# Optimization experiments

Hardware: AMD Instinct MI355X
Metric: run time of the kernel (lower is better)

Reference implementation:

```python
import jax, jax.numpy as jnp
import numpy as np


def _conv(x, w, b, pad):
    y = jax.lax.conv_general_dilated(x, w, window_strides=(1, 1),
                                     padding=[(pad, pad), (pad, pad)],
                                     dimension_numbers=('NCHW', 'OIHW', 'NCHW'))
    return y + b[None, :, None, None]


def _kernel_normalizer(mask, k):
    # softmax over the k*k kernel taps; hamming=1 so the renorm is a numerical no-op (kept faithful)
    n, mck2, h, w = mask.shape
    mc = mck2 // (k * k)
    m = jax.nn.softmax(mask.reshape(n, mc, k * k, h, w), axis=2)
    m = m / jnp.sum(m, axis=2, keepdims=True)
    return m.reshape(n, mck2, h, w)


def _carafe(feat, mask, k, g, s):
    # CARAFE: out[n,c,i,j] = sum_{ki,kj} mask[n, grp*k*k + ki*k + kj, i, j] * feat[n, c, i//s+ki-r, j//s+kj-r]
    n, c, h, w = feat.shape
    r = (k - 1) // 2
    cg = c // g
    hs, ws = h * s, w * s
    pad = jnp.pad(feat, ((0, 0), (0, 0), (r, r), (r, r)))
    m = mask.reshape(n, g, k * k, hs, ws)
    out = jnp.zeros((n, g, cg, hs, ws), feat.dtype)
    idx = 0
    for ki in range(k):
        for kj in range(k):
            sh = pad[:, :, ki:ki + h, kj:kj + w]
            if s > 1:
                sh = jnp.repeat(jnp.repeat(sh, s, axis=2), s, axis=3)
            out = out + sh.reshape(n, g, cg, hs, ws) * m[:, :, idx][:, :, None]
            idx += 1
    return out.reshape(n, c, hs, ws)


def setup_inputs() -> dict:
    key = jax.random.key(0)
    ks = jax.random.split(key, 8)
    N, CH, CL, H, W, CC = 4, 256, 256, 128, 128, 64
    KL, KH, EK = 5, 3, 3

    def w_init(k, shape):
        fan_in = shape[1] * shape[2] * shape[3]
        return jax.random.normal(k, shape, jnp.float32) * (1.0 / np.sqrt(fan_in))

    return {
        'hr_feat': jax.random.normal(ks[0], (N, CH, H, W), jnp.float32),
        'lr_feat': jax.random.normal(ks[1], (N, CL, H // 2, W // 2), jnp.float32),
        'hr_w': w_init(ks[2], (CC, CH, 1, 1)), 'hr_b': jnp.zeros((CC,), jnp.float32),
        'lr_w': w_init(ks[3], (CC, CL, 1, 1)), 'lr_b': jnp.zeros((CC,), jnp.float32),
        'enc_w': w_init(ks[4], (KL * KL, CC, EK, EK)), 'enc_b': jnp.zeros((KL * KL,), jnp.float32),
        'enc2_w': w_init(ks[5], (KH * KH, CC, EK, EK)), 'enc2_b': jnp.zeros((KH * KH,), jnp.float32),
    }


def reference(hr_feat, lr_feat, hr_w, hr_b, lr_w, lr_b, enc_w, enc_b, enc2_w, enc2_b):
    KL, KH, G = 5, 3, 1
    chf = _conv(hr_feat, hr_w, hr_b, 0)
    clf = _conv(lr_feat, lr_w, lr_b, 0)
    mask_hr_hr = _conv(chf, enc2_w, enc2_b, 1)
    mask_hr_init = _kernel_normalizer(mask_hr_hr, KH)
    chf = chf + chf - _carafe(chf, mask_hr_init, KH, G, 1)
    mask_lr_hr = _conv(chf, enc_w, enc_b, 1)
    mask_lr_init = _kernel_normalizer(mask_lr_hr, KL)
    mask_lr_lr_lr = _conv(clf, enc_w, enc_b, 1)
    # carafe scale-2 output is already hr-sized -> F.interpolate(nearest, hr size) is identity
    mask_lr_lr = _carafe(mask_lr_lr_lr, mask_lr_init, KL, G, 2)
    mask_lr = mask_lr_hr + mask_lr_lr
    mask_lr_init = _kernel_normalizer(mask_lr, KL)
    mask_hr_lr = _carafe(_conv(clf, enc2_w, enc2_b, 1), mask_lr_init, KL, G, 2)
    mask_hr = mask_hr_hr + mask_hr_lr
    mask_lr_out = _kernel_normalizer(mask_lr, KL)
    lr_out = _carafe(lr_feat, mask_lr_out, KL, G, 2)
    mask_hr_out = _kernel_normalizer(mask_hr, KH)
    hr_out = (hr_feat - _carafe(hr_feat, mask_hr_out, KH, G, 1)) + hr_feat
    return (mask_lr_out, hr_out, lr_out)
```

## Files before the change

### kernel.cpp

```cpp
#include <hip/hip_runtime.h>
#include <hip/hip_bf16.h>

typedef __hip_bfloat16 bf16;

constexpr int Nn  = 4;
constexpr int Ci  = 256;
constexpr int Cc  = 64;
constexpr int Hh  = 128;
constexpr int Ww  = 128;
constexpr int HWh = Hh * Ww;
constexpr int Hl  = 64;
constexpr int Wl  = 64;
constexpr int HWl = Hl * Wl;
constexpr int K2L = 25;
constexpr int K2H = 9;

constexpr size_t OFF_MASK = 0;
constexpr size_t OFF_HR   = (size_t)Nn * K2L * HWh;
constexpr size_t OFF_LR   = OFF_HR + (size_t)Nn * Ci * HWh;

constexpr size_t A_CHF    = 0;
constexpr size_t A_MLRHR  = 0;
constexpr size_t A_MLRLL  = 1700000;
constexpr size_t A_CLFE2  = 2200000;
constexpr size_t A_MLRS1  = 2400000;
constexpr size_t A_MHR2S  = 4100000;
constexpr size_t A_WHR    = 7800000;
constexpr size_t A_WLR    = 7820000;
constexpr size_t A_WENC   = 7840000;
constexpr size_t A_WENC2  = 7860000;
constexpr size_t A_BHR    = 7870000;
constexpr size_t A_BLR    = 7870100;
constexpr size_t A_BENC   = 7870200;
constexpr size_t A_BENC2  = 7870300;

constexpr size_t B_CLF    = 0;
constexpr size_t B_CHF2   = 1100000;
constexpr size_t B_MHRHR  = 5300000;
constexpr size_t B_MHRSM  = 5900000;
constexpr size_t B_MLR    = 0;
constexpr size_t B_MHR2   = 1700000;

__device__ __forceinline__ float tofloat(float v) { return v; }
__device__ __forceinline__ float tofloat(bf16 v) { return __bfloat162float(v); }

template<typename T> __device__ __forceinline__ T fromfloat(float v);
template<> __device__ __forceinline__ float fromfloat<float>(float v) { return v; }
template<> __device__ __forceinline__ bf16  fromfloat<bf16>(float v)  { return __float2bfloat16(v); }

__device__ __forceinline__ float* scrp(void* d, int f32, size_t reg, size_t off) {
  float* b = f32 ? ((float*)d + reg) : (float*)((bf16*)d + reg);
  return b + off;
}

__global__ void detect_dtype(const void* feat, int* flag) {
  __shared__ int s;
  if (threadIdx.x == 0) s = 0;
  __syncthreads();
  unsigned short b = ((const unsigned short*)feat)[threadIdx.x];
  float v = __uint_as_float(((unsigned int)b) << 16);
  if (!(fabsf(v) < 1000.0f)) atomicOr(&s, 1);
  __syncthreads();
  if (threadIdx.x == 0) *flag = s;
}

template<typename T>
__device__ void prep_body(const T* hw, const T* hb, const T* lw, const T* lb,
                          const T* ew, const T* eb, const T* e2w, const T* e2b,
                          float* whr, float* wlr, float* wenc, float* wenc2,
                          float* bhr, float* blr, float* benc, float* benc2) {
  int tid = blockIdx.x * 256 + threadIdx.x, nt = gridDim.x * 256;
  for (int i = tid; i < Cc * Ci; i += nt) {
    int co = i / Ci, ci = i % Ci;
    whr[ci * Cc + co] = tofloat(hw[i]);
    wlr[ci * Cc + co] = tofloat(lw[i]);
  }
  for (int i = tid; i < K2L * Cc * 9; i += nt) {
    int ko = i / (Cc * 9), r = i % (Cc * 9), ci = r / 9, k = r % 9;
    wenc[(ci * K2L + ko) * 9 + k] = tofloat(ew[i]);
  }
  for (int i = tid; i < K2H * Cc * 9; i += nt) {
    int ko = i / (Cc * 9), r = i % (Cc * 9), ci = r / 9, k = r % 9;
    wenc2[(ci * K2H + ko) * 9 + k] = tofloat(e2w[i]);
  }
  if (tid < Cc)  { bhr[tid] = tofloat(hb[tid]); blr[tid] = tofloat(lb[tid]); }
  if (tid < K2L) benc[tid]  = tofloat(eb[tid]);
  if (tid < K2H) benc2[tid] = tofloat(e2b[tid]);
}

__global__ void prep_weights(const int* flag, void* dout,
                             const void* hw, const void* hb, const void* lw, const void* lb,
                             const void* ew, const void* eb, const void* e2w, const void* e2b) {
  int f32 = *flag;
  float* whr   = scrp(dout, f32, OFF_LR, A_WHR);
  float* wlr   = scrp(dout, f32, OFF_LR, A_WLR);
  float* wenc  = scrp(dout, f32, OFF_LR, A_WENC);
  float* wenc2 = scrp(dout, f32, OFF_LR, A_WENC2);
  float* bhr   = scrp(dout, f32, OFF_LR, A_BHR);
  float* blr   = scrp(dout, f32, OFF_LR, A_BLR);
  float* benc  = scrp(dout, f32, OFF_LR, A_BENC);
  float* benc2 = scrp(dout, f32, OFF_LR, A_BENC2);
  if (f32) prep_body<float>((const float*)hw, (const float*)hb, (const float*)lw, (const float*)lb,
                            (const float*)ew, (const float*)eb, (const float*)e2w, (const float*)e2b,
                            whr, wlr, wenc, wenc2, bhr, blr, benc, benc2);
  else     prep_body<bf16>((const bf16*)hw, (const bf16*)hb, (const bf16*)lw, (const bf16*)lb,
                           (const bf16*)ew, (const bf16*)eb, (const bf16*)e2w, (const bf16*)e2b,
                           whr, wlr, wenc, wenc2, bhr, blr, benc, benc2);
}

template<typename T>
__device__ void conv1x1_body(const T* __restrict__ in, const float* __restrict__ wt,
                             const float* __restrict__ bias, float* __restrict__ out, int P) {
  const int tid = threadIdx.x;
  const int n = blockIdx.y;
  const int pbase = blockIdx.x * 64 + (tid & 63);
  const int co0 = __builtin_amdgcn_readfirstlane((tid >> 6) << 4);
  const T* inp = in + (size_t)n * Ci * P + pbase;

  float acc[16];
  #pragma unroll
  for (int c = 0; c < 16; ++c) acc[c] = bias[co0 + c];

  #pragma unroll 4
  for (int ci = 0; ci < Ci; ++ci) {
    float v = tofloat(inp[(size_t)ci * P]);
    const float* wr = wt + ci * Cc + co0;
    #pragma unroll
    for (int c = 0; c < 16; ++c) acc[c] = fmaf(v, wr[c], acc[c]);
  }
  float* op = out + (size_t)n * Cc * P + pbase;
  #pragma unroll
  for (int c = 0; c < 16; ++c) op[(size_t)(co0 + c) * P] = acc[c];
}

__global__ __launch_bounds__(256) void conv1x1_k(const int* flag, void* dout, const void* in,
                                                 size_t w_off, size_t b_off,
                                                 size_t o_reg, size_t o_off, int P) {
  int f32 = __builtin_amdgcn_readfirstlane(*flag);
  const float* wt   = scrp(dout, f32, OFF_LR, w_off);
  const float* bias = scrp(dout, f32, OFF_LR, b_off);
  float* out        = scrp(dout, f32, o_reg, o_off);
  if (f32) conv1x1_body<float>((const float*)in, wt, bias, out, P);
  else     conv1x1_body<bf16>((const bf16*)in, wt, bias, out, P);
}

template<int KO, int KOG>
__global__ __launch_bounds__(256) void conv3x3_k(const int* flag, void* dout,
                                                 size_t i_reg, size_t i_off,
                                                 size_t w_off, size_t b_off,
                                                 size_t o_reg, size_t o_off, int hh, int ww) {
  const int f32 = __builtin_amdgcn_readfirstlane(*flag);
  const float* in   = scrp(dout, f32, i_reg, i_off);
  const float* wt   = scrp(dout, f32, OFF_LR, w_off);
  const float* bias = scrp(dout, f32, OFF_LR, b_off);
  float* out        = scrp(dout, f32, o_reg, o_off);

  constexpr int NG = KO / KOG;
  __shared__ float tile[16 * 18 * 18];
  const int tid = threadIdx.x;
  const int tx = tid & 15, ty = tid >> 4;
  const int bx = blockIdx.x * 16, by = blockIdx.y * 16;
  const int n = blockIdx.z / NG;
  const int ko0 = (blockIdx.z % NG) * KOG;

  float acc[KOG];
  #pragma unroll
  for (int ko = 0; ko < KOG; ++ko) acc[ko] = bias[ko0 + ko];

  for (int cc = 0; cc < Cc; cc += 16) {
    __syncthreads();
    for (int i = tid; i < 16 * 18 * 18; i += 256) {
      int ci = i / 324, r = i % 324, yy = r / 18, xx = r % 18;
      int gy = by + yy - 1, gx = bx + xx - 1;
      float v = 0.f;
      if (gy >= 0 && gy < hh && gx >= 0 && gx < ww)
        v = in[(((size_t)n * Cc + cc + ci) * hh + gy) * ww + gx];
      tile[i] = v;
    }
    __syncthreads();
    for (int ci = 0; ci < 16; ++ci) {
      float nb[9];
      #pragma unroll
      for (int dy = 0; dy < 3; ++dy)
        #pragma unroll
        for (int dx = 0; dx < 3; ++dx)
          nb[dy * 3 + dx] = tile[ci * 324 + (ty + dy) * 18 + tx + dx];
      const float* wr = wt + ((size_t)(cc + ci) * KO + ko0) * 9;
      #pragma unroll
      for (int ko = 0; ko < KOG; ++ko)
        #pragma unroll
        for (int k = 0; k < 9; ++k)
          acc[ko] = fmaf(wr[ko * 9 + k], nb[k], acc[ko]);
    }
  }
  const size_t ob = (((size_t)n * KO + ko0) * hh + by + ty) * ww + bx + tx;
  #pragma unroll
  for (int ko = 0; ko < KOG; ++ko) out[ob + (size_t)ko * hh * ww] = acc[ko];
}

template<int K2>
__global__ __launch_bounds__(256) void softmax_k(const int* flag, void* dout,
                                                 size_t i_reg, size_t i_off,
                                                 int wf32, size_t o_reg, size_t o_off, int w0) {
  int f32 = __builtin_amdgcn_readfirstlane(*flag);
  const float* in = scrp(dout, f32, i_reg, i_off);
  const int p = blockIdx.x * blockDim.x + threadIdx.x;
  const int n = blockIdx.y;
  const float* ip = in + (size_t)n * K2 * HWh + p;
  float v[K2], m = -1e30f;
  #pragma unroll
  for (int k = 0; k < K2; ++k) { v[k] = ip[(size_t)k * HWh]; m = fmaxf(m, v[k]); }
  float s = 0.f;
  #pragma unroll
  for (int k = 0; k < K2; ++k) { v[k] = __expf(v[k] - m); s += v[k]; }
  const float inv = 1.0f / s;
  #pragma unroll
  for (int k = 0; k < K2; ++k) v[k] *= inv;

  if (wf32) {
    float* op = scrp(dout, f32, o_reg, o_off) + (size_t)n * K2 * HWh + p;
    #pragma unroll
    for (int k = 0; k < K2; ++k) op[(size_t)k * HWh] = v[k];
  }
  if (w0) {
    const size_t g = (size_t)n * K2 * HWh + p;
    if (f32) {
      float* o = (float*)dout;
      #pragma unroll
      for (int k = 0; k < K2; ++k) o[g + (size_t)k * HWh] = v[k];
    } else {
      bf16* o = (bf16*)dout;
      #pragma unroll
      for (int k = 0; k < K2; ++k) o[g + (size_t)k * HWh] = fromfloat<bf16>(v[k]);
    }
  }
}

template<typename FT, typename OT, int FINAL>
__device__ void carafe1_body(const FT* __restrict__ feat, const float* __restrict__ mask,
                             void* dout, size_t out_reg, float* outscr, int C, int CPB) {
  const int tid = threadIdx.x;
  const int tx = tid & 15, ty = tid >> 4;
  const int bx = blockIdx.x * 16, by = blockIdx.y * 16;
  const int numCG = C / CPB;
  const int n = blockIdx.z / numCG, cg = blockIdx.z % numCG;
  const int x = bx + tx, y = by + ty;

  float mv[9];
  #pragma unroll
  for (int k = 0; k < 9; ++k)
    mv[k] = mask[(((size_t)n * 9 + k) * Hh + y) * Ww + x];

  const int c0 = cg * CPB;
  for (int c = c0; c < c0 + CPB; ++c) {
    const FT* fp = feat + ((size_t)n * C + c) * HWh;
    float s = 0.f, center = 0.f;
    #pragma unroll
    for (int dy = -1; dy <= 1; ++dy)
      #pragma unroll
      for (int dx = -1; dx <= 1; ++dx) {
        int yy = y + dy, xx = x + dx;
        float fv = 0.f;
        if (yy >= 0 && yy < Hh && xx >= 0 && xx < Ww) fv = tofloat(fp[yy * Ww + xx]);
        if (dy == 0 && dx == 0) center = fv;
        s = fmaf(fv, mv[(dy + 1) * 3 + (dx + 1)], s);
      }
    float r = 2.f * center - s;
    const size_t li = ((size_t)n * C + c) * HWh + y * Ww + x;
    if (FINAL) ((OT*)dout)[out_reg + li] = fromfloat<OT>(r);
    else       outscr[li] = r;
  }
}

__global__ __launch_bounds__(256) void carafe1_scr_k(const int* flag, void* dout,
    size_t f_reg, size_t f_off, size_t m_reg, size_t m_off, size_t o_reg, size_t o_off,
    int C, int CPB) {
  int f32 = __builtin_amdgcn_readfirstlane(*flag);
  carafe1_body<float, float, 0>(scrp(dout, f32, f_reg, f_off), scrp(dout, f32, m_reg, m_off),
                                dout, 0, scrp(dout, f32, o_reg, o_off), C, CPB);
}

__global__ __launch_bounds__(256) void carafe1_io_k(const int* flag, void* dout, const void* feat,
    size_t m_reg, size_t m_off, size_t out_reg, int C, int CPB) {
  int f32 = __builtin_amdgcn_readfirstlane(*flag);
  const float* m = scrp(dout, f32, m_reg, m_off);
  if (f32) carafe1_body<float, float, 1>((const float*)feat, m, dout, out_reg, nullptr, C, CPB);
  else     carafe1_body<bf16, bf16, 1>((const bf16*)feat, m, dout, out_reg, nullptr, C, CPB);
}

template<typename FT, typename MT, typename OT, int ADD, int FINAL>
__device__ void carafe2_body(const FT* __restrict__ feat, const MT* __restrict__ mask,
                             const float* __restrict__ addend, void* dout, size_t out_reg,
                             float* outscr, int C, int CPB) {
  __shared__ float ft[8][144];
  const int tid = threadIdx.x;
  const int tx = tid & 15, ty = tid >> 4;
  const int bx = blockIdx.x * 16, by = blockIdx.y * 16;
  const int numCG = C / CPB;
  const int n = blockIdx.z / numCG, cg = blockIdx.z % numCG;
  const int x = bx + tx, y = by + ty;

  float mv[25];
  #pragma unroll
  for (int k = 0; k < 25; ++k)
    mv[k] = tofloat(mask[(((size_t)n * 25 + k) * Hh + y) * Ww + x]);

  const int fy0 = (by >> 1) - 2, fx0 = (bx >> 1) - 2;
  const int fyb = (ty >> 1) + 2, fxb = (tx >> 1) + 2;
  const int c0 = cg * CPB;

  for (int cb = 0; cb < CPB; cb += 8) {
    const int lim = (CPB - cb < 8) ? (CPB - cb) : 8;
    __syncthreads();
    for (int i = tid; i < lim * 144; i += 256) {
      int cc = i / 144, r = i % 144, fy = r / 12, fx = r % 12;
      int gy = fy0 + fy, gx = fx0 + fx;
      float v = 0.f;
      if (gy >= 0 && gy < Hl && gx >= 0 && gx < Wl)
        v = tofloat(feat[((size_t)n * C + c0 + cb + cc) * HWl + gy * Wl + gx]);
      ft[cc][r] = v;
    }
    __syncthreads();
    for (int cc = 0; cc < lim; ++cc) {
      float s = 0.f;
      #pragma unroll
      for (int ki = 0; ki < 5; ++ki)
        #pragma unroll
        for (int kj = 0; kj < 5; ++kj)
          s = fmaf(ft[cc][(fyb + ki - 2) * 12 + (fxb + kj - 2)], mv[ki * 5 + kj], s);
      const size_t li = (((size_t)n * C + c0 + cb + cc) * Hh + y) * Ww + x;
      float r = ADD ? (addend[li] + s) : s;
      if (FINAL) ((OT*)dout)[out_reg + li] = fromfloat<OT>(r);
      else       outscr[li] = r;
    }
  }
}

__global__ __launch_bounds__(256) void carafe2_scr_k(const int* flag, void* dout,
    size_t f_reg, size_t f_off, size_t m_reg, size_t m_off, size_t a_reg, size_t a_off,
    size_t o_reg, size_t o_off, int C, int CPB) {
  int f32 = __builtin_amdgcn_readfirstlane(*flag);
  carafe2_body<float, float, float, 1, 0>(scrp(dout, f32, f_reg, f_off), scrp(dout, f32, m_reg, m_off),
      scrp(dout, f32, a_reg, a_off), dout, 0, scrp(dout, f32, o_reg, o_off), C, CPB);
}

__global__ __launch_bounds__(256) void carafe2_m0_k(const int* flag, void* dout,
    size_t f_reg, size_t f_off, size_t a_reg, size_t a_off, size_t o_reg, size_t o_off,
    int C, int CPB) {
  int f32 = __builtin_amdgcn_readfirstlane(*flag);
  const float* f = scrp(dout, f32, f_reg, f_off);
  const float* a = scrp(dout, f32, a_reg, a_off);
  float* o = scrp(dout, f32, o_reg, o_off);
  if (f32) carafe2_body<float, float, float, 1, 0>(f, (const float*)dout, a, dout, 0, o, C, CPB);
  else     carafe2_body<float, bf16, float, 1, 0>(f, (const bf16*)dout, a, dout, 0, o, C, CPB);
}

__global__ __launch_bounds__(256) void carafe2_io_k(const int* flag, void* dout, const void* feat,
    size_t out_reg, int C, int CPB) {
  int f32 = __builtin_amdgcn_readfirstlane(*flag);
  if (f32) carafe2_body<float, float, float, 0, 1>((const float*)feat, (const float*)dout,
      nullptr, dout, out_reg, nullptr, C, CPB);
  else     carafe2_body<bf16, bf16, bf16, 0, 1>((const bf16*)feat, (const bf16*)dout,
      nullptr, dout, out_reg, nullptr, C, CPB);
}

extern "C" void kernel_launch(void* const* d_in, const int* in_sizes, int n_in,
                              void* d_out, int out_size, void* d_ws, size_t ws_size,
                              hipStream_t stream) {
  const void* hr_feat = d_in[0];
  const void* lr_feat = d_in[1];
  int* flag = (int*)d_ws;

  detect_dtype<<<1, 256, 0, stream>>>(hr_feat, flag);
  prep_weights<<<64, 256, 0, stream>>>(flag, d_out, d_in[2], d_in[3], d_in[4], d_in[5],
                                       d_in[6], d_in[7], d_in[8], d_in[9]);
  conv1x1_k<<<dim3(HWh / 64, Nn), 256, 0, stream>>>(flag, d_out, hr_feat, A_WHR, A_BHR, OFF_LR, A_CHF, HWh);
  conv1x1_k<<<dim3(HWl / 64, Nn), 256, 0, stream>>>(flag, d_out, lr_feat, A_WLR, A_BLR, OFF_HR, B_CLF, HWl);
  conv3x3_k<K2H, 3><<<dim3(8, 8, Nn * 3), 256, 0, stream>>>(flag, d_out, OFF_LR, A_CHF, A_WENC2, A_BENC2, OFF_HR, B_MHRHR, Hh, Ww);
  softmax_k<K2H><<<dim3(HWh / 128, Nn), 128, 0, stream>>>(flag, d_out, OFF_HR, B_MHRHR, 1, OFF_HR, B_MHRSM, 0);
  carafe1_scr_k<<<dim3(8, 8, Nn * (Cc / 16)), 256, 0, stream>>>(flag, d_out, OFF_LR, A_CHF, OFF_HR, B_MHRSM, OFF_HR, B_CHF2, Cc, 16);
  conv3x3_k<K2L, 5><<<dim3(8, 8, Nn * 5), 256, 0, stream>>>(flag, d_out, OFF_HR, B_CHF2, A_WENC, A_BENC, OFF_LR, A_MLRHR, Hh, Ww);
  conv3x3_k<K2L, 5><<<dim3(4, 4, Nn * 5), 256, 0, stream>>>(flag, d_out, OFF_HR, B_CLF, A_WENC, A_BENC, OFF_LR, A_MLRLL, Hl, Wl);
  conv3x3_k<K2H, 3><<<dim3(4, 4, Nn * 3), 256, 0, stream>>>(flag, d_out, OFF_HR, B_CLF, A_WENC2, A_BENC2, OFF_LR, A_CLFE2, Hl, Wl);
  softmax_k<K2L><<<dim3(HWh / 128, Nn), 128, 0, stream>>>(flag, d_out, OFF_LR, A_MLRHR, 1, OFF_LR, A_MLRS1, 0);
  carafe2_scr_k<<<dim3(8, 8, Nn * 5), 256, 0, stream>>>(flag, d_out, OFF_LR, A_MLRLL, OFF_LR, A_MLRS1,
                                                        OFF_LR, A_MLRHR, OFF_HR, B_MLR, K2L, 5);
  softmax_k<K2L><<<dim3(HWh / 128, Nn), 128, 0, stream>>>(flag, d_out, OFF_HR, B_MLR, 0, 0, 0, 1);
  carafe2_m0_k<<<dim3(8, 8, Nn * 3), 256, 0, stream>>>(flag, d_out, OFF_LR, A_CLFE2,
                                                       OFF_HR, B_MHRHR, OFF_HR, B_MHR2, K2H, 3);
  softmax_k<K2H><<<dim3(HWh / 128, Nn), 128, 0, stream>>>(flag, d_out, OFF_HR, B_MHR2, 1, OFF_LR, A_MHR2S, 0);
  carafe1_io_k<<<dim3(8, 8, Nn * (Ci / 32)), 256, 0, stream>>>(flag, d_out, hr_feat,
                                                               OFF_LR, A_MHR2S, OFF_HR, Ci, 32);
  carafe2_io_k<<<dim3(8, 8, Nn * (Ci / 32)), 256, 0, stream>>>(flag, d_out, lr_feat, OFF_LR, Ci, 32);
}
```

Baseline: 625.7 us.

## Fuse softmax into CARAFE kernels and merge low-res 3x3 convs

Three of the standalone softmax passes are removed. The softmax normalisation is now recomputed inside the carafe1 and carafe2 kernels, directly from the raw mask logits held in registers, which saves a round trip of the normalised masks through global memory and several kernel launches. The two low-resolution 3x3 encoder convolutions are merged into one launch that dispatches on the z block index. The low-res 1x1 conv is split across more blocks to raise parallelism. In exchange, every channel-group block of the carafe kernels repeats the exp/normalise work on the mask values.

```diff
diff --git a/kernel.cpp b/kernel.cpp
--- a/kernel.cpp
+++ b/kernel.cpp
@@ -23,8 +23,7 @@
 constexpr size_t A_MLRHR  = 0;
 constexpr size_t A_MLRLL  = 1700000;
 constexpr size_t A_CLFE2  = 2200000;
-constexpr size_t A_MLRS1  = 2400000;
-constexpr size_t A_MHR2S  = 4100000;
+constexpr size_t A_MHRRAW = 4100000;
 constexpr size_t A_WHR    = 7800000;
 constexpr size_t A_WLR    = 7820000;
 constexpr size_t A_WENC   = 7840000;
@@ -37,9 +36,7 @@
 constexpr size_t B_CLF    = 0;
 constexpr size_t B_CHF2   = 1100000;
 constexpr size_t B_MHRHR  = 5300000;
-constexpr size_t B_MHRSM  = 5900000;
 constexpr size_t B_MLR    = 0;
-constexpr size_t B_MHR2   = 1700000;
 
 __device__ __forceinline__ float tofloat(float v) { return v; }
 __device__ __forceinline__ float tofloat(bf16 v) { return __bfloat162float(v); }
@@ -108,31 +105,32 @@
                            whr, wlr, wenc, wenc2, bhr, blr, benc, benc2);
 }
 
-template<typename T>
+template<typename T, int CW>
 __device__ void conv1x1_body(const T* __restrict__ in, const float* __restrict__ wt,
                              const float* __restrict__ bias, float* __restrict__ out, int P) {
   const int tid = threadIdx.x;
-  const int n = blockIdx.y;
+  const int n = blockIdx.z;
   const int pbase = blockIdx.x * 64 + (tid & 63);
-  const int co0 = __builtin_amdgcn_readfirstlane((tid >> 6) << 4);
+  const int co0 = __builtin_amdgcn_readfirstlane(blockIdx.y * 4 * CW + ((tid >> 6) * CW));
   const T* inp = in + (size_t)n * Ci * P + pbase;
 
-  float acc[16];
-  #pragma unroll
-  for (int c = 0; c < 16; ++c) acc[c] = bias[co0 + c];
+  float acc[CW];
+  #pragma unroll
+  for (int c = 0; c < CW; ++c) acc[c] = bias[co0 + c];
 
   #pragma unroll 4
   for (int ci = 0; ci < Ci; ++ci) {
     float v = tofloat(inp[(size_t)ci * P]);
     const float* wr = wt + ci * Cc + co0;
     #pragma unroll
-    for (int c = 0; c < 16; ++c) acc[c] = fmaf(v, wr[c], acc[c]);
+    for (int c = 0; c < CW; ++c) acc[c] = fmaf(v, wr[c], acc[c]);
   }
   float* op = out + (size_t)n * Cc * P + pbase;
   #pragma unroll
-  for (int c = 0; c < 16; ++c) op[(size_t)(co0 + c) * P] = acc[c];
-}
-
+  for (int c = 0; c < CW; ++c) op[(size_t)(co0 + c) * P] = acc[c];
+}
+
+template<int CW>
 __global__ __launch_bounds__(256) void conv1x1_k(const int* flag, void* dout, const void* in,
                                                  size_t w_off, size_t b_off,
                                                  size_t o_reg, size_t o_off, int P) {
@@ -140,28 +138,19 @@
   const float* wt   = scrp(dout, f32, OFF_LR, w_off);
   const float* bias = scrp(dout, f32, OFF_LR, b_off);
   float* out        = scrp(dout, f32, o_reg, o_off);
-  if (f32) conv1x1_body<float>((const float*)in, wt, bias, out, P);
-  else     conv1x1_body<bf16>((const bf16*)in, wt, bias, out, P);
+  if (f32) conv1x1_body<float, CW>((const float*)in, wt, bias, out, P);
+  else     conv1x1_body<bf16, CW>((const bf16*)in, wt, bias, out, P);
 }
 
 template<int KO, int KOG>
-__global__ __launch_bounds__(256) void conv3x3_k(const int* flag, void* dout,
-                                                 size_t i_reg, size_t i_off,
-                                                 size_t w_off, size_t b_off,
-                                                 size_t o_reg, size_t o_off, int hh, int ww) {
-  const int f32 = __builtin_amdgcn_readfirstlane(*flag);
-  const float* in   = scrp(dout, f32, i_reg, i_off);
-  const float* wt   = scrp(dout, f32, OFF_LR, w_off);
-  const float* bias = scrp(dout, f32, OFF_LR, b_off);
-  float* out        = scrp(dout, f32, o_reg, o_off);
-
-  constexpr int NG = KO / KOG;
-  __shared__ float tile[16 * 18 * 18];
+__device__ __forceinline__ void conv3x3_body(const float* __restrict__ in,
+                                             const float* __restrict__ wt,
+                                             const float* __restrict__ bias,
+                                             float* __restrict__ out,
+                                             int hh, int ww, int n, int ko0, float* tile) {
   const int tid = threadIdx.x;
   const int tx = tid & 15, ty = tid >> 4;
   const int bx = blockIdx.x * 16, by = blockIdx.y * 16;
-  const int n = blockIdx.z / NG;
-  const int ko0 = (blockIdx.z % NG) * KOG;
 
   float acc[KOG];
   #pragma unroll
@@ -198,10 +187,44 @@
   for (int ko = 0; ko < KOG; ++ko) out[ob + (size_t)ko * hh * ww] = acc[ko];
 }
 
+template<int KO, int KOG>
+__global__ __launch_bounds__(256) void conv3x3_k(const int* flag, void* dout,
+                                                 size_t i_reg, size_t i_off,
+                                                 size_t w_off, size_t b_off,
+                                                 size_t o_reg, size_t o_off, int hh, int ww) {
+  const int f32 = __builtin_amdgcn_readfirstlane(*flag);
+  const float* in   = scrp(dout, f32, i_reg, i_off);
+  const float* wt   = scrp(dout, f32, OFF_LR, w_off);
+  const float* bias = scrp(dout, f32, OFF_LR, b_off);
+  float* out        = scrp(dout, f32, o_reg, o_off);
+
+  constexpr int NG = KO / KOG;
+  __shared__ float tile[16 * 18 * 18];
+  const int n = blockIdx.z / NG;
+  const int ko0 = (blockIdx.z % NG) * KOG;
+  conv3x3_body<KO, KOG>(in, wt, bias, out, hh, ww, n, ko0, tile);
+}
+
+__global__ __launch_bounds__(256) void conv3x3_dual_k(const int* flag, void* dout) {
+  const int f32 = __builtin_amdgcn_readfirstlane(*flag);
+  const float* in    = scrp(dout, f32, OFF_HR, B_CLF);
+  const float* wenc  = scrp(dout, f32, OFF_LR, A_WENC);
+  const float* benc  = scrp(dout, f32, OFF_LR, A_BENC);
+  const float* wenc2 = scrp(dout, f32, OFF_LR, A_WENC2);
+  const float* benc2 = scrp(dout, f32, OFF_LR, A_BENC2);
+  float* out_ll  = scrp(dout, f32, OFF_LR, A_MLRLL);
+  float* out_e2  = scrp(dout, f32, OFF_LR, A_CLFE2);
+
+  __shared__ float tile[16 * 18 * 18];
+  const int g = blockIdx.z % 8;
+  const int n = blockIdx.z / 8;
+  if (g < 5) conv3x3_body<K2L, 5>(in, wenc, benc, out_ll, Hl, Wl, n, g * 5, tile);
+  else       conv3x3_body<K2H, 3>(in, wenc2, benc2, out_e2, Hl, Wl, n, (g - 5) * 3, tile);
+}
+
 template<int K2>
 __global__ __launch_bounds__(256) void softmax_k(const int* flag, void* dout,
-                                                 size_t i_reg, size_t i_off,
-                                                 int wf32, size_t o_reg, size_t o_off, int w0) {
+                                                 size_t i_reg, size_t i_off) {
   int f32 = __builtin_amdgcn_readfirstlane(*flag);
   const float* in = scrp(dout, f32, i_reg, i_off);
   const int p = blockIdx.x * blockDim.x + threadIdx.x;
@@ -217,26 +240,19 @@
   #pragma unroll
   for (int k = 0; k < K2; ++k) v[k] *= inv;
 
-  if (wf32) {
-    float* op = scrp(dout, f32, o_reg, o_off) + (size_t)n * K2 * HWh + p;
-    #pragma unroll
-    for (int k = 0; k < K2; ++k) op[(size_t)k * HWh] = v[k];
-  }
-  if (w0) {
-    const size_t g = (size_t)n * K2 * HWh + p;
-    if (f32) {
-      float* o = (float*)dout;
-      #pragma unroll
-      for (int k = 0; k < K2; ++k) o[g + (size_t)k * HWh] = v[k];
-    } else {
-      bf16* o = (bf16*)dout;
-      #pragma unroll
-      for (int k = 0; k < K2; ++k) o[g + (size_t)k * HWh] = fromfloat<bf16>(v[k]);
-    }
-  }
-}
-
-template<typename FT, typename OT, int FINAL>
+  const size_t g = (size_t)n * K2 * HWh + p;
+  if (f32) {
+    float* o = (float*)dout;
+    #pragma unroll
+    for (int k = 0; k < K2; ++k) o[g + (size_t)k * HWh] = v[k];
+  } else {
+    bf16* o = (bf16*)dout;
+    #pragma unroll
+    for (int k = 0; k < K2; ++k) o[g + (size_t)k * HWh] = fromfloat<bf16>(v[k]);
+  }
+}
+
+template<typename FT, typename OT, int FINAL, int SM>
 __device__ void carafe1_body(const FT* __restrict__ feat, const float* __restrict__ mask,
                              void* dout, size_t out_reg, float* outscr, int C, int CPB) {
   const int tid = threadIdx.x;
@@ -250,6 +266,17 @@
   #pragma unroll
   for (int k = 0; k < 9; ++k)
     mv[k] = mask[(((size_t)n * 9 + k) * Hh + y) * Ww + x];
+  if (SM) {
+    float m = -1e30f;
+    #pragma unroll
+    for (int k = 0; k < 9; ++k) m = fmaxf(m, mv[k]);
+    float s = 0.f;
+    #pragma unroll
+    for (int k = 0; k < 9; ++k) { mv[k] = __expf(mv[k] - m); s += mv[k]; }
+    const float inv = 1.0f / s;
+    #pragma unroll
+    for (int k = 0; k < 9; ++k) mv[k] *= inv;
+  }
 
   const int c0 = cg * CPB;
   for (int c = c0; c < c0 + CPB; ++c) {
@@ -276,19 +303,19 @@
     size_t f_reg, size_t f_off, size_t m_reg, size_t m_off, size_t o_reg, size_t o_off,
     int C, int CPB) {
   int f32 = __builtin_amdgcn_readfirstlane(*flag);
-  carafe1_body<float, float, 0>(scrp(dout, f32, f_reg, f_off), scrp(dout, f32, m_reg, m_off),
-                                dout, 0, scrp(dout, f32, o_reg, o_off), C, CPB);
+  carafe1_body<float, float, 0, 1>(scrp(dout, f32, f_reg, f_off), scrp(dout, f32, m_reg, m_off),
+                                   dout, 0, scrp(dout, f32, o_reg, o_off), C, CPB);
 }
 
 __global__ __launch_bounds__(256) void carafe1_io_k(const int* flag, void* dout, const void* feat,
     size_t m_reg, size_t m_off, size_t out_reg, int C, int CPB) {
   int f32 = __builtin_amdgcn_readfirstlane(*flag);
   const float* m = scrp(dout, f32, m_reg, m_off);
-  if (f32) carafe1_body<float, float, 1>((const float*)feat, m, dout, out_reg, nullptr, C, CPB);
-  else     carafe1_body<bf16, bf16, 1>((const bf16*)feat, m, dout, out_reg, nullptr, C, CPB);
-}
-
-template<typename FT, typename MT, typename OT, int ADD, int FINAL>
+  if (f32) carafe1_body<float, float, 1, 1>((const float*)feat, m, dout, out_reg, nullptr, C, CPB);
+  else     carafe1_body<bf16, bf16, 1, 1>((const bf16*)feat, m, dout, out_reg, nullptr, C, CPB);
+}
+
+template<typename FT, typename MT, typename OT, int ADD, int FINAL, int SM>
 __device__ void carafe2_body(const FT* __restrict__ feat, const MT* __restrict__ mask,
                              const float* __restrict__ addend, void* dout, size_t out_reg,
                              float* outscr, int C, int CPB) {
@@ -304,6 +331,17 @@
   #pragma unroll
   for (int k = 0; k < 25; ++k)
     mv[k] = tofloat(mask[(((size_t)n * 25 + k) * Hh + y) * Ww + x]);
+  if (SM) {
+    float m = -1e30f;
+    #pragma unroll
+    for (int k = 0; k < 25; ++k) m = fmaxf(m, mv[k]);
+    float s = 0.f;
+    #pragma unroll
+    for (int k = 0; k < 25; ++k) { mv[k] = __expf(mv[k] - m); s += mv[k]; }
+    const float inv = 1.0f / s;
+    #pragma unroll
+    for (int k = 0; k < 25; ++k) mv[k] *= inv;
+  }
 
   const int fy0 = (by >> 1) - 2, fx0 = (bx >> 1) - 2;
   const int fyb = (ty >> 1) + 2, fxb = (tx >> 1) + 2;
@@ -340,7 +378,7 @@
     size_t f_reg, size_t f_off, size_t m_reg, size_t m_off, size_t a_reg, size_t a_off,
     size_t o_reg, size_t o_off, int C, int CPB) {
   int f32 = __builtin_amdgcn_readfirstlane(*flag);
-  carafe2_body<float, float, float, 1, 0>(scrp(dout, f32, f_reg, f_off), scrp(dout, f32, m_reg, m_off),
+  carafe2_body<float, float, float, 1, 0, 1>(scrp(dout, f32, f_reg, f_off), scrp(dout, f32, m_reg, m_off),
       scrp(dout, f32, a_reg, a_off), dout, 0, scrp(dout, f32, o_reg, o_off), C, CPB);
 }
 
@@ -351,16 +389,16 @@
   const float* f = scrp(dout, f32, f_reg, f_off);
   const float* a = scrp(dout, f32, a_reg, a_off);
   float* o = scrp(dout, f32, o_reg, o_off);
-  if (f32) carafe2_body<float, float, float, 1, 0>(f, (const float*)dout, a, dout, 0, o, C, CPB);
-  else     carafe2_body<float, bf16, float, 1, 0>(f, (const bf16*)dout, a, dout, 0, o, C, CPB);
+  if (f32) carafe2_body<float, float, float, 1, 0, 0>(f, (const float*)dout, a, dout, 0, o, C, CPB);
+  else     carafe2_body<float, bf16, float, 1, 0, 0>(f, (const bf16*)dout, a, dout, 0, o, C, CPB);
 }
 
 __global__ __launch_bounds__(256) void carafe2_io_k(const int* flag, void* dout, const void* feat,
     size_t out_reg, int C, int CPB) {
   int f32 = __builtin_amdgcn_readfirstlane(*flag);
-  if (f32) carafe2_body<float, float, float, 0, 1>((const float*)feat, (const float*)dout,
+  if (f32) carafe2_body<float, float, float, 0, 1, 0>((const float*)feat, (const float*)dout,
       nullptr, dout, out_reg, nullptr, C, CPB);
-  else     carafe2_body<bf16, bf16, bf16, 0, 1>((const bf16*)feat, (const bf16*)dout,
+  else     carafe2_body<bf16, bf16, bf16, 0, 1, 0>((const bf16*)feat, (const bf16*)dout,
       nullptr, dout, out_reg, nullptr, C, CPB);
 }
 
@@ -374,22 +412,18 @@
   detect_dtype<<<1, 256, 0, stream>>>(hr_feat, flag);
   prep_weights<<<64, 256, 0, stream>>>(flag, d_out, d_in[2], d_in[3], d_in[4], d_in[5],
                                        d_in[6], d_in[7], d_in[8], d_in[9]);
-  conv1x1_k<<<dim3(HWh / 64, Nn), 256, 0, stream>>>(flag, d_out, hr_feat, A_WHR, A_BHR, OFF_LR, A_CHF, HWh);
-  conv1x1_k<<<dim3(HWl / 64, Nn), 256, 0, stream>>>(flag, d_out, lr_feat, A_WLR, A_BLR, OFF_HR, B_CLF, HWl);
+  conv1x1_k<16><<<dim3(HWh / 64, 1, Nn), 256, 0, stream>>>(flag, d_out, hr_feat, A_WHR, A_BHR, OFF_LR, A_CHF, HWh);
+  conv1x1_k<8><<<dim3(HWl / 64, 2, Nn), 256, 0, stream>>>(flag, d_out, lr_feat, A_WLR, A_BLR, OFF_HR, B_CLF, HWl);
   conv3x3_k<K2H, 3><<<dim3(8, 8, Nn * 3), 256, 0, stream>>>(flag, d_out, OFF_LR, A_CHF, A_WENC2, A_BENC2, OFF_HR, B_MHRHR, Hh, Ww);
-  softmax_k<K2H><<<dim3(HWh / 128, Nn), 128, 0, stream>>>(flag, d_out, OFF_HR, B_MHRHR, 1, OFF_HR, B_MHRSM, 0);
-  carafe1_scr_k<<<dim3(8, 8, Nn * (Cc / 16)), 256, 0, stream>>>(flag, d_out, OFF_LR, A_CHF, OFF_HR, B_MHRSM, OFF_HR, B_CHF2, Cc, 16);
+  carafe1_scr_k<<<dim3(8, 8, Nn * (Cc / 16)), 256, 0, stream>>>(flag, d_out, OFF_LR, A_CHF, OFF_HR, B_MHRHR, OFF_HR, B_CHF2, Cc, 16);
   conv3x3_k<K2L, 5><<<dim3(8, 8, Nn * 5), 256, 0, stream>>>(flag, d_out, OFF_HR, B_CHF2, A_WENC, A_BENC, OFF_LR, A_MLRHR, Hh, Ww);
-  conv3x3_k<K2L, 5><<<dim3(4, 4, Nn * 5), 256, 0, stream>>>(flag, d_out, OFF_HR, B_CLF, A_WENC, A_BENC, OFF_LR, A_MLRLL, Hl, Wl);
-  conv3x3_k<K2H, 3><<<dim3(4, 4, Nn * 3), 256, 0, stream>>>(flag, d_out, OFF_HR, B_CLF, A_WENC2, A_BENC2, OFF_LR, A_CLFE2, Hl, Wl);
-  softmax_k<K2L><<<dim3(HWh / 128, Nn), 128, 0, stream>>>(flag, d_out, OFF_LR, A_MLRHR, 1, OFF_LR, A_MLRS1, 0);
-  carafe2_scr_k<<<dim3(8, 8, Nn * 5), 256, 0, stream>>>(flag, d_out, OFF_LR, A_MLRLL, OFF_LR, A_MLRS1,
+  conv3x3_dual_k<<<dim3(4, 4, Nn * 8), 256, 0, stream>>>(flag, d_out);
+  carafe2_scr_k<<<dim3(8, 8, Nn * 5), 256, 0, stream>>>(flag, d_out, OFF_LR, A_MLRLL, OFF_LR, A_MLRHR,
                                                         OFF_LR, A_MLRHR, OFF_HR, B_MLR, K2L, 5);
-  softmax_k<K2L><<<dim3(HWh / 128, Nn), 128, 0, stream>>>(flag, d_out, OFF_HR, B_MLR, 0, 0, 0, 1);
+  softmax_k<K2L><<<dim3(HWh / 128, Nn), 128, 0, stream>>>(flag, d_out, OFF_HR, B_MLR);
   carafe2_m0_k<<<dim3(8, 8, Nn * 3), 256, 0, stream>>>(flag, d_out, OFF_LR, A_CLFE2,
-                                                       OFF_HR, B_MHRHR, OFF_HR, B_MHR2, K2H, 3);
-  softmax_k<K2H><<<dim3(HWh / 128, Nn), 128, 0, stream>>>(flag, d_out, OFF_HR, B_MHR2, 1, OFF_LR, A_MHR2S, 0);
+                                                       OFF_HR, B_MHRHR, OFF_LR, A_MHRRAW, K2H, 3);
   carafe1_io_k<<<dim3(8, 8, Nn * (Ci / 32)), 256, 0, stream>>>(flag, d_out, hr_feat,
-                                                               OFF_LR, A_MHR2S, OFF_HR, Ci, 32);
+                                                               OFF_LR, A_MHRRAW, OFF_HR, Ci, 32);
   carafe2_io_k<<<dim3(8, 8, Nn * (Ci / 32)), 256, 0, stream>>>(flag, d_out, lr_feat, OFF_LR, Ci, 32);
 }
```

Result: faster. 575.7 us (-8.0%).
